# Kernel tuning notes

Measured on AMD Instinct MI355X. Metric: run time of the kernel, lower is better.

## Reference

```python
import jax, jax.numpy as jnp
import numpy as np
from jax.scipy.special import logsumexp

EPSILON = 0.01        # temperature
DIST_THRESH = 0.2
NUM_ITERS = 3
NEG_INF = -1.0e9

B, N, M, C = 4, 4096, 4096, 256


def setup_inputs() -> dict:
    key = jax.random.key(0)
    k1, k2, k3, k4, k5 = jax.random.split(key, 5)
    source_feats = jax.random.normal(k1, (B, N, C), dtype=jnp.float32)
    source_locs = jax.random.uniform(k2, (B, N, 2), dtype=jnp.float32)
    target_locs = jax.random.uniform(k3, (B, M, 2), dtype=jnp.float32)
    source_valid_mask = jax.random.bernoulli(k4, 0.9, (B, N))
    target_valid_mask = jax.random.bernoulli(k5, 0.9, (B, M))
    return {
        "source_feats": source_feats,
        "source_locs": source_locs,
        "target_locs": target_locs,
        "source_valid_mask": source_valid_mask,
        "target_valid_mask": target_valid_mask,
    }


def reference(source_feats, source_locs, target_locs, source_valid_mask, target_valid_mask):
    # pairwise squared distances: [B, M, N]
    diff = target_locs[:, :, None, :] - source_locs[:, None, :, :]  # [B, M, N, 2]
    dist_sq = jnp.sum(diff * diff, axis=-1)                          # [B, M, N]
    log_K = -dist_sq / (EPSILON + 1e-8)

    valid_connection = dist_sq < (DIST_THRESH ** 2)
    valid_connection = valid_connection & source_valid_mask[:, None, :]
    valid_connection = valid_connection & target_valid_mask[:, :, None]
    log_K = jnp.where(valid_connection, log_K, NEG_INF)

    # Sinkhorn iterations in log space
    v = jnp.zeros((log_K.shape[0], 1, log_K.shape[2]), dtype=log_K.dtype)  # [B,1,N]
    u = jnp.zeros((log_K.shape[0], log_K.shape[1], 1), dtype=log_K.dtype)  # [B,M,1]
    for _ in range(NUM_ITERS):
        u = -logsumexp(log_K + v, axis=2, keepdims=True)
        v = -logsumexp(log_K + u, axis=1, keepdims=True)
        v = jnp.where(source_valid_mask[:, None, :], v, 0.0)

    attn = jnp.exp(log_K + u + v)  # [B, M, N]
    attn = jax.lax.stop_gradient(attn)  # original computes it under torch.no_grad

    target_feats = jnp.einsum('bmn,bnc->bmc', attn, source_feats)
    target_feats = target_feats * target_valid_mask[:, :, None].astype(target_feats.dtype)
    has_source = jnp.any(valid_connection, axis=-1, keepdims=True)
    target_feats = target_feats * has_source.astype(target_feats.dtype)
    return target_feats
```

## Files before the change

kernel.cpp:

```cpp
#include <hip/hip_runtime.h>
#include <math.h>

#define BB 4
#define BN 4096
#define CC 256
constexpr float T2      = 0.04f;
constexpr float INV_EPS = (float)(1.0 / 0.01000001);

typedef __attribute__((ext_vector_type(8)))  short bf16x8;
typedef __attribute__((ext_vector_type(16))) float f32x16;

__device__ __forceinline__ int cell_of(float x, float y) {
  int cx = (int)(x * 5.0f); cx = cx < 0 ? 0 : (cx > 4 ? 4 : cx);
  int cy = (int)(y * 5.0f); cy = cy < 0 ? 0 : (cy > 4 ? 4 : cy);
  return cy * 5 + cx;
}

__device__ __forceinline__ void dma16(const void* g, void* l) {
  __builtin_amdgcn_global_load_lds(
      (const __attribute__((address_space(1))) void*)g,
      (__attribute__((address_space(3))) void*)l, 16, 0, 0);
}
__device__ __forceinline__ void dma4(const void* g, void* l) {
  __builtin_amdgcn_global_load_lds(
      (const __attribute__((address_space(1))) void*)g,
      (__attribute__((address_space(3))) void*)l, 4, 0, 0);
}

__global__ __launch_bounds__(256) void k_bin(
    const float* __restrict__ tlocs, const float* __restrict__ slocs,
    const int* __restrict__ tmask, const int* __restrict__ smask,
    int* __restrict__ Zc,
    int* __restrict__ starts_t, int* __restrict__ starts_s,
    int* __restrict__ perm_t, int* __restrict__ perm_s,
    float4* __restrict__ t_sorted, float4* __restrict__ s_sorted) {
  const int which = blockIdx.x & 1, b = blockIdx.x >> 1;
  const float* locs = which ? slocs : tlocs;
  const int*   mask = which ? smask : tmask;
  int* starts       = which ? starts_s : starts_t;
  int* perm         = which ? perm_s : perm_t;
  float4* pack      = which ? s_sorted : t_sorted;
  const int tid = threadIdx.x;
  if (blockIdx.x == 0) Zc[tid] = 0;
  __shared__ int cnt[25];
  __shared__ int st[26];
  __shared__ int cur[25];
  if (tid < 25) cnt[tid] = 0;
  __syncthreads();
  for (int i = tid; i < BN; i += 256)
    atomicAdd(&cnt[cell_of(locs[(b * BN + i) * 2], locs[(b * BN + i) * 2 + 1])], 1);
  __syncthreads();
  if (tid == 0) {
    int acc = 0;
    for (int c = 0; c < 25; c++) { st[c] = acc; acc += cnt[c]; }
    st[25] = acc;
  }
  __syncthreads();
  if (tid < 25) cur[tid] = st[tid];
  if (tid < 26) starts[b * 32 + tid] = st[tid];
  __syncthreads();
  for (int i = tid; i < BN; i += 256) {
    float x = locs[(b * BN + i) * 2], y = locs[(b * BN + i) * 2 + 1];
    int pos = atomicAdd(&cur[cell_of(x, y)], 1);
    perm[b * BN + pos] = i;
    pack[b * BN + pos] = make_float4(x, y, 0.f, mask[b * BN + i] ? 1.f : 0.f);
  }
}

__global__ __launch_bounds__(256) void k_pack(
    const float* __restrict__ feats, const int* __restrict__ perm_s,
    unsigned* __restrict__ fB) {
  const int b   = blockIdx.x >> 8;
  const int blk = blockIdx.x & 255;
  const int tid = threadIdx.x;
  __shared__ float fs[16][260];
  __shared__ int   sidx[16];
  if (tid < 16) sidx[tid] = perm_s[b * BN + blk * 16 + tid];
  __syncthreads();
  #pragma unroll
  for (int q = 0; q < 4; q++) {
    int idx = q * 256 + tid;
    int r = idx >> 6, c4 = idx & 63;
    float4 v = ((const float4*)feats)[(((b << 12) + sidx[r]) << 6) + c4];
    fs[r][c4 * 4 + 0] = v.x; fs[r][c4 * 4 + 1] = v.y;
    fs[r][c4 * 4 + 2] = v.z; fs[r][c4 * 4 + 3] = v.w;
  }
  __syncthreads();
  const int ch = tid;
  unsigned* dst = fB + ((((size_t)b << 8) + blk) << 12) + ch * 16;
  unsigned pk[16];
  #pragma unroll
  for (int sl = 0; sl < 16; sl++) {
    float f = fs[sl][ch];
    unsigned fb = __float_as_uint(f);
    unsigned hb = fb & 0xFFFF0000u;
    float lo = f - __uint_as_float(hb);
    pk[sl ^ (((ch >> 1) & 3) << 2)] = hb | (__float_as_uint(lo) >> 16);
  }
  #pragma unroll
  for (int q = 0; q < 4; q++)
    ((uint4*)dst)[q] = make_uint4(pk[q*4], pk[q*4+1], pk[q*4+2], pk[q*4+3]);
}

__global__ __launch_bounds__(256) void k_sink(const float4* __restrict__ opp,
                                              float4* __restrict__ own,
                                              const int* __restrict__ opp_starts,
                                              const int* __restrict__ Zin,
                                              int* __restrict__ Zout,
                                              int zero_invalid) {
  const int wv   = threadIdx.x >> 6;
  const int lane = threadIdx.x & 63;
  const int rowb = blockIdx.x * 16 + wv * 4;
  const int b    = rowb >> 12;
  float4 me[4];
  float  s[4] = {0.f, 0.f, 0.f, 0.f};
  int ryLo = 5, ryHi = -1, rxLo = 5, rxHi = -1;
  #pragma unroll
  for (int i = 0; i < 4; i++) {
    me[i] = own[rowb + i];
    if (me[i].w != 0.f) {
      int cell = cell_of(me[i].x, me[i].y);
      int cy = cell / 5, cx = cell % 5;
      ryLo = min(ryLo, max(cy - 1, 0)); ryHi = max(ryHi, min(cy + 1, 4));
      rxLo = min(rxLo, max(cx - 1, 0)); rxHi = max(rxHi, min(cx + 1, 4));
    }
  }
  for (int ry = ryLo; ry <= ryHi; ry++) {
    const int r0 = opp_starts[b * 32 + ry * 5 + rxLo];
    const int r1 = opp_starts[b * 32 + ry * 5 + rxHi + 1];
    for (int j = r0 + lane; j < r1; j += 64) {
      float4 o = opp[b * BN + j];
      #pragma unroll
      for (int i = 0; i < 4; i++) {
        float dx = me[i].x - o.x, dy = me[i].y - o.y;
        float d2 = fmaf(dx, dx, dy * dy);
        bool  c  = (d2 < T2) && (o.w != 0.f) && (me[i].w != 0.f);
        float t  = c ? fmaf(d2, -INV_EPS, o.z) : -3e30f;
        s[i] += __expf(t);
      }
    }
  }
  #pragma unroll
  for (int i = 0; i < 4; i++)
    for (int off = 32; off > 0; off >>= 1) s[i] += __shfl_xor(s[i], off);
  if (lane == 0) {
    const float Zf = (float)Zin[b];
    #pragma unroll
    for (int i = 0; i < 4; i++) {
      float ss  = s[i] + Zf;
      float val = (ss > 0.f) ? -logf(ss) : 1.0e9f;
      if (zero_invalid && me[i].w == 0.f) val = 0.f;
      own[rowb + i] = make_float4(me[i].x, me[i].y, val, me[i].w);
      if (val == 1.0e9f) atomicAdd(&Zout[b], 1);
    }
  }
}

#define MAXCH 12
#define BUFU  4352

__global__ __launch_bounds__(256) void k_out(
    const unsigned* __restrict__ fB, const float4* __restrict__ t_sorted,
    const float4* __restrict__ s_sorted, const int* __restrict__ perm_t,
    const int* __restrict__ starts_t, const int* __restrict__ starts_s,
    float* __restrict__ out) {
  const int b = blockIdx.z;
  const int cell = blockIdx.y / 3, rsel = blockIdx.y % 3;
  const int cy = cell / 5, cx = cell % 5;
  const int ry = cy + rsel - 1;
  if (ry < 0 || ry > 4) return;
  const int t0 = starts_t[b * 32 + cell], t1 = starts_t[b * 32 + cell + 1];
  const int base = t0 + blockIdx.x * 32;
  if (base >= t1) return;
  const int rx0 = max(cx - 1, 0), rx1 = min(cx + 1, 4);
  const int s0 = starts_s[b * 32 + ry * 5 + rx0];
  const int s1 = starts_s[b * 32 + ry * 5 + rx1 + 1];
  if (s0 >= s1) return;
  const int nt = min(32, t1 - base);

  __shared__ __align__(16) unsigned pool[3 * BUFU];
  __shared__ float4 tL[32];
  __shared__ int    morg[32];

  const int tid  = threadIdx.x;
  const int lane = tid & 63;
  const int w    = tid >> 6;

  if (tid < 32) {
    if (tid < nt) {
      tL[tid]   = t_sorted[b * BN + base + tid];
      morg[tid] = perm_t[b * BN + base + tid];
    } else {
      tL[tid]   = make_float4(0.f, 0.f, 0.f, 0.f);
      morg[tid] = 0;
    }
  }
  __syncthreads();

  const int kg = lane >> 5;
  const int ln = lane & 31;
  const float4 t4a = tL[ln];
  const int sB = b * BN;

  const int blk0 = s0 >> 4;
  const int nBlk = ((s1 + 15) >> 4) - blk0;

  const unsigned* fBb = fB + (((size_t)b) << 20);
  auto ISSUE = [&](int t, int bufI) {
    const unsigned* g = fBb + ((size_t)t << 12);
    unsigned* lb = pool + bufI * BUFU;
    #pragma unroll
    for (int q = 0; q < 4; q++)
      dma16(g + (w * 4 + q) * 256 + lane * 4, (void*)(lb + (w * 4 + q) * 256));
    dma4((const char*)s_sorted + ((size_t)(sB + t * 16) << 4) + lane * 4,
         (void*)(lb + 4096 + w * 64));
  };

  ISSUE(blk0, 0);
  ISSUE(blk0 + min(1, nBlk - 1), 1);

  f32x16 acc0, acc1;
  #pragma unroll
  for (int i = 0; i < 16; i++) { acc0[i] = 0.f; acc1[i] = 0.f; }

  int cur = 0;
  for (int r = 0; r < nBlk; r++) {
    asm volatile("s_waitcnt vmcnt(5)" ::: "memory");
    __builtin_amdgcn_sched_barrier(0);
    ISSUE(blk0 + min(r + 2, nBlk - 1), cur == 0 ? 2 : cur - 1);
    const unsigned* tile = pool + cur * BUFU;
    const int j0 = (blk0 + r) * 16 + kg * 8;
    unsigned ahv[8], alv[8];
    #pragma unroll
    for (int e = 0; e < 8; e++) {
      float4 s4 = *(const float4*)(tile + 4096 + w * 64 + (kg * 8 + e) * 4);
      int j = j0 + e;
      float dx = t4a.x - s4.x, dy = t4a.y - s4.y;
      float d2 = fmaf(dx, dx, dy * dy);
      bool  c  = (j >= s0) && (j < s1) && (d2 < T2) &&
                 (s4.w != 0.f) && (t4a.w != 0.f);
      float a  = c ? __expf(fmaf(d2, -INV_EPS, t4a.z + s4.z)) : 0.f;
      unsigned ab = __float_as_uint(a);
      unsigned hb = ab & 0xFFFF0000u;
      float alo = a - __uint_as_float(hb);
      ahv[e] = ab >> 16;
      alv[e] = __float_as_uint(alo) >> 16;
    }
    union { unsigned u[4]; bf16x8 v; } BH, BL;
    #pragma unroll
    for (int i = 0; i < 4; i++) {
      BH.u[i] = ahv[2*i] | (ahv[2*i+1] << 16);
      BL.u[i] = alv[2*i] | (alv[2*i+1] << 16);
    }
    #pragma unroll
    for (int mt = 0; mt < 2; mt++) {
      const int chl = w * 64 + mt * 32 + ln;
      const int xv  = (chl >> 1) & 3;
      const int g0  = ((kg << 1) | 0) ^ xv;
      const int g1  = ((kg << 1) | 1) ^ xv;
      union { uint4 q[2]; unsigned u[8]; } A;
      A.q[0] = *(const uint4*)(tile + chl * 16 + g0 * 4);
      A.q[1] = *(const uint4*)(tile + chl * 16 + g1 * 4);
      union { unsigned u[4]; bf16x8 v; } AH, AL;
      #pragma unroll
      for (int i = 0; i < 4; i++) {
        AH.u[i] = (A.u[2*i] >> 16)     | (A.u[2*i+1] & 0xFFFF0000u);
        AL.u[i] = (A.u[2*i] & 0xFFFFu) | (A.u[2*i+1] << 16);
      }
      if (mt == 0) {
        acc0 = __builtin_amdgcn_mfma_f32_32x32x16_bf16(AH.v, BH.v, acc0, 0, 0, 0);
        acc0 = __builtin_amdgcn_mfma_f32_32x32x16_bf16(AH.v, BL.v, acc0, 0, 0, 0);
        acc0 = __builtin_amdgcn_mfma_f32_32x32x16_bf16(AL.v, BH.v, acc0, 0, 0, 0);
      } else {
        acc1 = __builtin_amdgcn_mfma_f32_32x32x16_bf16(AH.v, BH.v, acc1, 0, 0, 0);
        acc1 = __builtin_amdgcn_mfma_f32_32x32x16_bf16(AH.v, BL.v, acc1, 0, 0, 0);
        acc1 = __builtin_amdgcn_mfma_f32_32x32x16_bf16(AL.v, BH.v, acc1, 0, 0, 0);
      }
    }
    cur = (cur == 2) ? 0 : cur + 1;
  }

  asm volatile("s_waitcnt vmcnt(0)" ::: "memory");
  __syncthreads();
  float* Dl = (float*)pool;
  #pragma unroll
  for (int mt = 0; mt < 2; mt++) {
    #pragma unroll
    for (int rg = 0; rg < 4; rg++) {
      int chb = w * 64 + mt * 32 + 8 * rg + 4 * kg;
      float4 v;
      if (mt == 0) v = make_float4(acc0[rg*4], acc0[rg*4+1], acc0[rg*4+2], acc0[rg*4+3]);
      else         v = make_float4(acc1[rg*4], acc1[rg*4+1], acc1[rg*4+2], acc1[rg*4+3]);
      *(float4*)&Dl[ln * 268 + chb] = v;
    }
  }
  __syncthreads();
  {
    const int tmg = tid >> 5, chg = tid & 31;
    #pragma unroll
    for (int i = 0; i < 4; i++) {
      int tm = tmg * 4 + i;
      if (tm < nt) {
        float* op = out + (((b << 12) + morg[tm]) << 8) + chg * 4;
        float4 d0 = *(float4*)&Dl[tm * 268 + chg * 4];
        float4 d1 = *(float4*)&Dl[tm * 268 + 128 + chg * 4];
        atomicAdd(op + 0, d0.x); atomicAdd(op + 1, d0.y);
        atomicAdd(op + 2, d0.z); atomicAdd(op + 3, d0.w);
        atomicAdd(op + 128, d1.x); atomicAdd(op + 129, d1.y);
        atomicAdd(op + 130, d1.z); atomicAdd(op + 131, d1.w);
      }
    }
  }
}

extern "C" void kernel_launch(void* const* d_in, const int* in_sizes, int n_in,
                              void* d_out, int out_size, void* d_ws, size_t ws_size,
                              hipStream_t stream) {
  const float* feats = (const float*)d_in[0];
  const float* slocs = (const float*)d_in[1];
  const float* tlocs = (const float*)d_in[2];
  const int*   smask = (const int*)d_in[3];
  const int*   tmask = (const int*)d_in[4];
  float* out = (float*)d_out;

  char* ws = (char*)d_ws;
  int*    Zc       = (int*)(ws + 1024);
  int*    starts_t = (int*)(ws + 2048);
  int*    starts_s = (int*)(ws + 2560);
  int*    perm_t   = (int*)(ws + 4096);
  int*    perm_s   = (int*)(ws + 69632);
  float4* s_sorted = (float4*)(ws + 135168);
  float4* t_sorted = (float4*)(ws + 397312);
  unsigned* fB     = (unsigned*)(ws + 663552);

  hipMemsetAsync(out, 0, (size_t)out_size * sizeof(float), stream);
  k_bin<<<8, 256, 0, stream>>>(tlocs, slocs, tmask, smask, Zc,
                               starts_t, starts_s, perm_t, perm_s,
                               t_sorted, s_sorted);
  k_pack<<<1024, 256, 0, stream>>>(feats, perm_s, fB);
  for (int it = 0; it < 3; it++) {
    k_sink<<<1024, 256, 0, stream>>>(s_sorted, t_sorted, starts_s,
                                     Zc + (it == 0 ? 0 : (2 * it) * 4),
                                     Zc + (2 * it + 1) * 4, 0);
    k_sink<<<1024, 256, 0, stream>>>(t_sorted, s_sorted, starts_t,
                                     Zc + (2 * it + 1) * 4,
                                     Zc + (2 * it + 2) * 4, 1);
  }
  k_out<<<dim3(MAXCH, 75, BB), 256, 0, stream>>>(fB, t_sorted, s_sorted,
                                                 perm_t, starts_t, starts_s,
                                                 out);
}
```

Baseline: 558.8 us.

## Use persistent work-queue k_out with 64-target tiles and simplify k_pack

k_out now processes 64 targets per work item with four accumulators, so each loaded source feature tile feeds twice as many MFMAs. It runs as a persistent grid of 768 blocks that take items from an atomic queue counter reset in k_bin, replacing the sparse 3D grid that had many early-exit blocks. k_pack drops its LDS staging and reads features directly. In exchange, register pressure rises, the output path adds an extra LDS round and barrier, and the queue serializes on one global atomic.

After: 552.9 us. Within noise of the previous version (-1.1%).

```diff
diff --git a/kernel.cpp b/kernel.cpp
--- a/kernel.cpp
+++ b/kernel.cpp
@@ -30,7 +30,7 @@
 __global__ __launch_bounds__(256) void k_bin(
     const float* __restrict__ tlocs, const float* __restrict__ slocs,
     const int* __restrict__ tmask, const int* __restrict__ smask,
-    int* __restrict__ Zc,
+    int* __restrict__ Zc, int* __restrict__ qcnt,
     int* __restrict__ starts_t, int* __restrict__ starts_s,
     int* __restrict__ perm_t, int* __restrict__ perm_s,
     float4* __restrict__ t_sorted, float4* __restrict__ s_sorted) {
@@ -41,7 +41,10 @@
   int* perm         = which ? perm_s : perm_t;
   float4* pack      = which ? s_sorted : t_sorted;
   const int tid = threadIdx.x;
-  if (blockIdx.x == 0) Zc[tid] = 0;
+  if (blockIdx.x == 0) {
+    Zc[tid] = 0;
+    if (tid == 0) qcnt[0] = 0;
+  }
   __shared__ int cnt[25];
   __shared__ int st[26];
   __shared__ int cur[25];
@@ -73,30 +76,20 @@
   const int b   = blockIdx.x >> 8;
   const int blk = blockIdx.x & 255;
   const int tid = threadIdx.x;
-  __shared__ float fs[16][260];
-  __shared__ int   sidx[16];
+  __shared__ int sidx[16];
   if (tid < 16) sidx[tid] = perm_s[b * BN + blk * 16 + tid];
   __syncthreads();
-  #pragma unroll
-  for (int q = 0; q < 4; q++) {
-    int idx = q * 256 + tid;
-    int r = idx >> 6, c4 = idx & 63;
-    float4 v = ((const float4*)feats)[(((b << 12) + sidx[r]) << 6) + c4];
-    fs[r][c4 * 4 + 0] = v.x; fs[r][c4 * 4 + 1] = v.y;
-    fs[r][c4 * 4 + 2] = v.z; fs[r][c4 * 4 + 3] = v.w;
-  }
-  __syncthreads();
   const int ch = tid;
-  unsigned* dst = fB + ((((size_t)b << 8) + blk) << 12) + ch * 16;
   unsigned pk[16];
   #pragma unroll
   for (int sl = 0; sl < 16; sl++) {
-    float f = fs[sl][ch];
-    unsigned fb = __float_as_uint(f);
-    unsigned hb = fb & 0xFFFF0000u;
+    float f = feats[((((size_t)(b << 12)) + sidx[sl]) << 8) + ch];
+    unsigned fbt = __float_as_uint(f);
+    unsigned hb  = fbt & 0xFFFF0000u;
     float lo = f - __uint_as_float(hb);
     pk[sl ^ (((ch >> 1) & 3) << 2)] = hb | (__float_as_uint(lo) >> 16);
   }
+  unsigned* dst = fB + ((((size_t)b << 8) + blk) << 12) + ch * 16;
   #pragma unroll
   for (int q = 0; q < 4; q++)
     ((uint4*)dst)[q] = make_uint4(pk[q*4], pk[q*4+1], pk[q*4+2], pk[q*4+3]);
@@ -156,159 +149,187 @@
   }
 }
 
-#define MAXCH 12
-#define BUFU  4352
+#define BUFU   4352
+#define NITEMS (BB * 25 * 3 * 6)
 
 __global__ __launch_bounds__(256) void k_out(
     const unsigned* __restrict__ fB, const float4* __restrict__ t_sorted,
     const float4* __restrict__ s_sorted, const int* __restrict__ perm_t,
     const int* __restrict__ starts_t, const int* __restrict__ starts_s,
-    float* __restrict__ out) {
-  const int b = blockIdx.z;
-  const int cell = blockIdx.y / 3, rsel = blockIdx.y % 3;
-  const int cy = cell / 5, cx = cell % 5;
-  const int ry = cy + rsel - 1;
-  if (ry < 0 || ry > 4) return;
-  const int t0 = starts_t[b * 32 + cell], t1 = starts_t[b * 32 + cell + 1];
-  const int base = t0 + blockIdx.x * 32;
-  if (base >= t1) return;
-  const int rx0 = max(cx - 1, 0), rx1 = min(cx + 1, 4);
-  const int s0 = starts_s[b * 32 + ry * 5 + rx0];
-  const int s1 = starts_s[b * 32 + ry * 5 + rx1 + 1];
-  if (s0 >= s1) return;
-  const int nt = min(32, t1 - base);
-
+    int* __restrict__ qcnt, float* __restrict__ out) {
   __shared__ __align__(16) unsigned pool[3 * BUFU];
-  __shared__ float4 tL[32];
-  __shared__ int    morg[32];
+  __shared__ float4 tL[64];
+  __shared__ int qi;
 
   const int tid  = threadIdx.x;
   const int lane = tid & 63;
   const int w    = tid >> 6;
-
-  if (tid < 32) {
-    if (tid < nt) {
-      tL[tid]   = t_sorted[b * BN + base + tid];
-      morg[tid] = perm_t[b * BN + base + tid];
-    } else {
-      tL[tid]   = make_float4(0.f, 0.f, 0.f, 0.f);
-      morg[tid] = 0;
-    }
-  }
-  __syncthreads();
-
-  const int kg = lane >> 5;
-  const int ln = lane & 31;
-  const float4 t4a = tL[ln];
-  const int sB = b * BN;
-
-  const int blk0 = s0 >> 4;
-  const int nBlk = ((s1 + 15) >> 4) - blk0;
-
-  const unsigned* fBb = fB + (((size_t)b) << 20);
-  auto ISSUE = [&](int t, int bufI) {
-    const unsigned* g = fBb + ((size_t)t << 12);
-    unsigned* lb = pool + bufI * BUFU;
+  const int kg   = lane >> 5;
+  const int ln   = lane & 31;
+
+  for (;;) {
+    if (tid == 0) qi = atomicAdd(qcnt, 1);
+    __syncthreads();
+    const int item = qi;
+    __syncthreads();
+    if (item >= NITEMS) break;
+    const int b    = item / 450;
+    const int r1_  = item % 450;
+    const int cell = r1_ / 18;
+    const int r2_  = r1_ % 18;
+    const int rsel = r2_ / 6, pair = r2_ % 6;
+    const int cy = cell / 5, cx = cell % 5;
+    const int ry = cy + rsel - 1;
+    if (ry < 0 || ry > 4) continue;
+    const int t0 = starts_t[b * 32 + cell], t1 = starts_t[b * 32 + cell + 1];
+    const int base = t0 + pair * 64;
+    if (base >= t1) continue;
+    const int rx0 = max(cx - 1, 0), rx1 = min(cx + 1, 4);
+    const int s0 = starts_s[b * 32 + ry * 5 + rx0];
+    const int s1 = starts_s[b * 32 + ry * 5 + rx1 + 1];
+    if (s0 >= s1) continue;
+    const int nt = min(64, t1 - base);
+
+    if (tid < 64)
+      tL[tid] = (tid < nt) ? t_sorted[b * BN + base + tid]
+                           : make_float4(0.f, 0.f, 0.f, 0.f);
+    __syncthreads();
+    const float4 t4a0 = tL[ln];
+    const float4 t4a1 = tL[32 + ln];
+    const int sB = b * BN;
+    const int blk0 = s0 >> 4;
+    const int nBlk = ((s1 + 15) >> 4) - blk0;
+
+    const unsigned* fBb = fB + (((size_t)b) << 20);
+    auto ISSUE = [&](int t, int bufI) {
+      const unsigned* g = fBb + ((size_t)t << 12);
+      unsigned* lb = pool + bufI * BUFU;
+      #pragma unroll
+      for (int q = 0; q < 4; q++)
+        dma16(g + (w * 4 + q) * 256 + lane * 4, (void*)(lb + (w * 4 + q) * 256));
+      dma4((const char*)s_sorted + ((size_t)(sB + t * 16) << 4) + lane * 4,
+           (void*)(lb + 4096 + w * 64));
+    };
+    ISSUE(blk0, 0);
+    ISSUE(blk0 + min(1, nBlk - 1), 1);
+
+    f32x16 a00, a01, a10, a11;
     #pragma unroll
-    for (int q = 0; q < 4; q++)
-      dma16(g + (w * 4 + q) * 256 + lane * 4, (void*)(lb + (w * 4 + q) * 256));
-    dma4((const char*)s_sorted + ((size_t)(sB + t * 16) << 4) + lane * 4,
-         (void*)(lb + 4096 + w * 64));
-  };
-
-  ISSUE(blk0, 0);
-  ISSUE(blk0 + min(1, nBlk - 1), 1);
-
-  f32x16 acc0, acc1;
-  #pragma unroll
-  for (int i = 0; i < 16; i++) { acc0[i] = 0.f; acc1[i] = 0.f; }
-
-  int cur = 0;
-  for (int r = 0; r < nBlk; r++) {
-    asm volatile("s_waitcnt vmcnt(5)" ::: "memory");
-    __builtin_amdgcn_sched_barrier(0);
-    ISSUE(blk0 + min(r + 2, nBlk - 1), cur == 0 ? 2 : cur - 1);
-    const unsigned* tile = pool + cur * BUFU;
-    const int j0 = (blk0 + r) * 16 + kg * 8;
-    unsigned ahv[8], alv[8];
+    for (int i = 0; i < 16; i++) { a00[i] = 0.f; a01[i] = 0.f; a10[i] = 0.f; a11[i] = 0.f; }
+
+    int cur = 0;
+    for (int r = 0; r < nBlk; r++) {
+      asm volatile("s_waitcnt vmcnt(5)" ::: "memory");
+      __builtin_amdgcn_sched_barrier(0);
+      ISSUE(blk0 + min(r + 2, nBlk - 1), cur == 0 ? 2 : cur - 1);
+      const unsigned* tile = pool + cur * BUFU;
+      const int j0 = (blk0 + r) * 16 + kg * 8;
+      unsigned ah0[8], al0[8], ah1[8], al1[8];
+      #pragma unroll
+      for (int e = 0; e < 8; e++) {
+        float4 s4 = *(const float4*)(tile + 4096 + w * 64 + (kg * 8 + e) * 4);
+        int j = j0 + e;
+        bool inr = (j >= s0) && (j < s1) && (s4.w != 0.f);
+        float dx0 = t4a0.x - s4.x, dy0 = t4a0.y - s4.y;
+        float d20 = fmaf(dx0, dx0, dy0 * dy0);
+        bool  c0  = inr && (d20 < T2) && (t4a0.w != 0.f);
+        float a0  = c0 ? __expf(fmaf(d20, -INV_EPS, t4a0.z + s4.z)) : 0.f;
+        unsigned ab0 = __float_as_uint(a0);
+        unsigned hb0 = ab0 & 0xFFFF0000u;
+        float alo0 = a0 - __uint_as_float(hb0);
+        ah0[e] = ab0 >> 16; al0[e] = __float_as_uint(alo0) >> 16;
+        float dx1 = t4a1.x - s4.x, dy1 = t4a1.y - s4.y;
+        float d21 = fmaf(dx1, dx1, dy1 * dy1);
+        bool  c1  = inr && (d21 < T2) && (t4a1.w != 0.f);
+        float a1  = c1 ? __expf(fmaf(d21, -INV_EPS, t4a1.z + s4.z)) : 0.f;
+        unsigned ab1 = __float_as_uint(a1);
+        unsigned hb1 = ab1 & 0xFFFF0000u;
+        float alo1 = a1 - __uint_as_float(hb1);
+        ah1[e] = ab1 >> 16; al1[e] = __float_as_uint(alo1) >> 16;
+      }
+      union { unsigned u[4]; bf16x8 v; } BH0, BL0, BH1, BL1;
+      #pragma unroll
+      for (int i = 0; i < 4; i++) {
+        BH0.u[i] = ah0[2*i] | (ah0[2*i+1] << 16);
+        BL0.u[i] = al0[2*i] | (al0[2*i+1] << 16);
+        BH1.u[i] = ah1[2*i] | (ah1[2*i+1] << 16);
+        BL1.u[i] = al1[2*i] | (al1[2*i+1] << 16);
+      }
+      #pragma unroll
+      for (int mt = 0; mt < 2; mt++) {
+        const int chl = w * 64 + mt * 32 + ln;
+        const int xv  = (chl >> 1) & 3;
+        const int g0  = ((kg << 1) | 0) ^ xv;
+        const int g1  = ((kg << 1) | 1) ^ xv;
+        union { uint4 q[2]; unsigned u[8]; } A;
+        A.q[0] = *(const uint4*)(tile + chl * 16 + g0 * 4);
+        A.q[1] = *(const uint4*)(tile + chl * 16 + g1 * 4);
+        union { unsigned u[4]; bf16x8 v; } AH, AL;
+        #pragma unroll
+        for (int i = 0; i < 4; i++) {
+          AH.u[i] = (A.u[2*i] >> 16)     | (A.u[2*i+1] & 0xFFFF0000u);
+          AL.u[i] = (A.u[2*i] & 0xFFFFu) | (A.u[2*i+1] << 16);
+        }
+        if (mt == 0) {
+          a00 = __builtin_amdgcn_mfma_f32_32x32x16_bf16(AH.v, BH0.v, a00, 0, 0, 0);
+          a00 = __builtin_amdgcn_mfma_f32_32x32x16_bf16(AH.v, BL0.v, a00, 0, 0, 0);
+          a00 = __builtin_amdgcn_mfma_f32_32x32x16_bf16(AL.v, BH0.v, a00, 0, 0, 0);
+          a10 = __builtin_amdgcn_mfma_f32_32x32x16_bf16(AH.v, BH1.v, a10, 0, 0, 0);
+          a10 = __builtin_amdgcn_mfma_f32_32x32x16_bf16(AH.v, BL1.v, a10, 0, 0, 0);
+          a10 = __builtin_amdgcn_mfma_f32_32x32x16_bf16(AL.v, BH1.v, a10, 0, 0, 0);
+        } else {
+          a01 = __builtin_amdgcn_mfma_f32_32x32x16_bf16(AH.v, BH0.v, a01, 0, 0, 0);
+          a01 = __builtin_amdgcn_mfma_f32_32x32x16_bf16(AH.v, BL0.v, a01, 0, 0, 0);
+          a01 = __builtin_amdgcn_mfma_f32_32x32x16_bf16(AL.v, BH0.v, a01, 0, 0, 0);
+          a11 = __builtin_amdgcn_mfma_f32_32x32x16_bf16(AH.v, BH1.v, a11, 0, 0, 0);
+          a11 = __builtin_amdgcn_mfma_f32_32x32x16_bf16(AH.v, BL1.v, a11, 0, 0, 0);
+          a11 = __builtin_amdgcn_mfma_f32_32x32x16_bf16(AL.v, BH1.v, a11, 0, 0, 0);
+        }
+      }
+      cur = (cur == 2) ? 0 : cur + 1;
+    }
+
+    asm volatile("s_waitcnt vmcnt(0)" ::: "memory");
+    __syncthreads();
+    float* Dl = (float*)pool;
     #pragma unroll
-    for (int e = 0; e < 8; e++) {
-      float4 s4 = *(const float4*)(tile + 4096 + w * 64 + (kg * 8 + e) * 4);
-      int j = j0 + e;
-      float dx = t4a.x - s4.x, dy = t4a.y - s4.y;
-      float d2 = fmaf(dx, dx, dy * dy);
-      bool  c  = (j >= s0) && (j < s1) && (d2 < T2) &&
-                 (s4.w != 0.f) && (t4a.w != 0.f);
-      float a  = c ? __expf(fmaf(d2, -INV_EPS, t4a.z + s4.z)) : 0.f;
-      unsigned ab = __float_as_uint(a);
-      unsigned hb = ab & 0xFFFF0000u;
-      float alo = a - __uint_as_float(hb);
-      ahv[e] = ab >> 16;
-      alv[e] = __float_as_uint(alo) >> 16;
-    }
-    union { unsigned u[4]; bf16x8 v; } BH, BL;
-    #pragma unroll
-    for (int i = 0; i < 4; i++) {
-      BH.u[i] = ahv[2*i] | (ahv[2*i+1] << 16);
-      BL.u[i] = alv[2*i] | (alv[2*i+1] << 16);
-    }
-    #pragma unroll
-    for (int mt = 0; mt < 2; mt++) {
-      const int chl = w * 64 + mt * 32 + ln;
-      const int xv  = (chl >> 1) & 3;
-      const int g0  = ((kg << 1) | 0) ^ xv;
-      const int g1  = ((kg << 1) | 1) ^ xv;
-      union { uint4 q[2]; unsigned u[8]; } A;
-      A.q[0] = *(const uint4*)(tile + chl * 16 + g0 * 4);
-      A.q[1] = *(const uint4*)(tile + chl * 16 + g1 * 4);
-      union { unsigned u[4]; bf16x8 v; } AH, AL;
-      #pragma unroll
-      for (int i = 0; i < 4; i++) {
-        AH.u[i] = (A.u[2*i] >> 16)     | (A.u[2*i+1] & 0xFFFF0000u);
-        AL.u[i] = (A.u[2*i] & 0xFFFFu) | (A.u[2*i+1] << 16);
-      }
-      if (mt == 0) {
-        acc0 = __builtin_amdgcn_mfma_f32_32x32x16_bf16(AH.v, BH.v, acc0, 0, 0, 0);
-        acc0 = __builtin_amdgcn_mfma_f32_32x32x16_bf16(AH.v, BL.v, acc0, 0, 0, 0);
-        acc0 = __builtin_amdgcn_mfma_f32_32x32x16_bf16(AL.v, BH.v, acc0, 0, 0, 0);
-      } else {
-        acc1 = __builtin_amdgcn_mfma_f32_32x32x16_bf16(AH.v, BH.v, acc1, 0, 0, 0);
-        acc1 = __builtin_amdgcn_mfma_f32_32x32x16_bf16(AH.v, BL.v, acc1, 0, 0, 0);
-        acc1 = __builtin_amdgcn_mfma_f32_32x32x16_bf16(AL.v, BH.v, acc1, 0, 0, 0);
-      }
-    }
-    cur = (cur == 2) ? 0 : cur + 1;
-  }
-
-  asm volatile("s_waitcnt vmcnt(0)" ::: "memory");
-  __syncthreads();
-  float* Dl = (float*)pool;
-  #pragma unroll
-  for (int mt = 0; mt < 2; mt++) {
-    #pragma unroll
-    for (int rg = 0; rg < 4; rg++) {
-      int chb = w * 64 + mt * 32 + 8 * rg + 4 * kg;
-      float4 v;
-      if (mt == 0) v = make_float4(acc0[rg*4], acc0[rg*4+1], acc0[rg*4+2], acc0[rg*4+3]);
-      else         v = make_float4(acc1[rg*4], acc1[rg*4+1], acc1[rg*4+2], acc1[rg*4+3]);
-      *(float4*)&Dl[ln * 268 + chb] = v;
-    }
-  }
-  __syncthreads();
-  {
-    const int tmg = tid >> 5, chg = tid & 31;
-    #pragma unroll
-    for (int i = 0; i < 4; i++) {
-      int tm = tmg * 4 + i;
-      if (tm < nt) {
-        float* op = out + (((b << 12) + morg[tm]) << 8) + chg * 4;
-        float4 d0 = *(float4*)&Dl[tm * 268 + chg * 4];
-        float4 d1 = *(float4*)&Dl[tm * 268 + 128 + chg * 4];
-        atomicAdd(op + 0, d0.x); atomicAdd(op + 1, d0.y);
-        atomicAdd(op + 2, d0.z); atomicAdd(op + 3, d0.w);
-        atomicAdd(op + 128, d1.x); atomicAdd(op + 129, d1.y);
-        atomicAdd(op + 130, d1.z); atomicAdd(op + 131, d1.w);
-      }
+    for (int c = 0; c < 2; c++) {
+      #pragma unroll
+      for (int mt = 0; mt < 2; mt++) {
+        #pragma unroll
+        for (int rg = 0; rg < 4; rg++) {
+          int chb = w * 64 + mt * 32 + 8 * rg + 4 * kg;
+          float4 v;
+          if (c == 0) {
+            if (mt == 0) v = make_float4(a00[rg*4], a00[rg*4+1], a00[rg*4+2], a00[rg*4+3]);
+            else         v = make_float4(a01[rg*4], a01[rg*4+1], a01[rg*4+2], a01[rg*4+3]);
+          } else {
+            if (mt == 0) v = make_float4(a10[rg*4], a10[rg*4+1], a10[rg*4+2], a10[rg*4+3]);
+            else         v = make_float4(a11[rg*4], a11[rg*4+1], a11[rg*4+2], a11[rg*4+3]);
+          }
+          *(float4*)&Dl[ln * 268 + chb] = v;
+        }
+      }
+      __syncthreads();
+      {
+        const int tmg = tid >> 5, chg = tid & 31;
+        #pragma unroll
+        for (int i = 0; i < 4; i++) {
+          int tm = tmg * 4 + i;
+          int gt = c * 32 + tm;
+          if (gt < nt) {
+            int row = perm_t[sB + base + gt];
+            float* op = out + (((b << 12) + row) << 8) + chg * 4;
+            float4 d0 = *(float4*)&Dl[tm * 268 + chg * 4];
+            float4 d1 = *(float4*)&Dl[tm * 268 + 128 + chg * 4];
+            atomicAdd(op + 0, d0.x); atomicAdd(op + 1, d0.y);
+            atomicAdd(op + 2, d0.z); atomicAdd(op + 3, d0.w);
+            atomicAdd(op + 128, d1.x); atomicAdd(op + 129, d1.y);
+            atomicAdd(op + 130, d1.z); atomicAdd(op + 131, d1.w);
+          }
+        }
+      }
+      __syncthreads();
     }
   }
 }
@@ -324,6 +345,7 @@
   float* out = (float*)d_out;
 
   char* ws = (char*)d_ws;
+  int*    qcnt     = (int*)(ws);
   int*    Zc       = (int*)(ws + 1024);
   int*    starts_t = (int*)(ws + 2048);
   int*    starts_s = (int*)(ws + 2560);
@@ -334,7 +356,7 @@
   unsigned* fB     = (unsigned*)(ws + 663552);
 
   hipMemsetAsync(out, 0, (size_t)out_size * sizeof(float), stream);
-  k_bin<<<8, 256, 0, stream>>>(tlocs, slocs, tmask, smask, Zc,
+  k_bin<<<8, 256, 0, stream>>>(tlocs, slocs, tmask, smask, Zc, qcnt,
                                starts_t, starts_s, perm_t, perm_s,
                                t_sorted, s_sorted);
   k_pack<<<1024, 256, 0, stream>>>(feats, perm_s, fB);
@@ -346,7 +368,6 @@
                                      Zc + (2 * it + 1) * 4,
                                      Zc + (2 * it + 2) * 4, 1);
   }
-  k_out<<<dim3(MAXCH, 75, BB), 256, 0, stream>>>(fB, t_sorted, s_sorted,
-                                                 perm_t, starts_t, starts_s,
-                                                 out);
-}
+  k_out<<<768, 256, 0, stream>>>(fB, t_sorted, s_sorted, perm_t,
+                                 starts_t, starts_s, qcnt, out);
+}
```

## Make k_out a persistent work-queue kernel with direct register loads of features

Applied to the files above, without the earlier changes.

k_out becomes a persistent kernel: 1024 blocks pull work items from an atomic counter that k_bin resets. Feature tiles are now loaded from global memory straight into registers with one-tile register prefetch, replacing the LDS triple buffer filled by global_load_lds. k_pack drops its LDS staging and XOR swizzle and reads features directly. The goal is less LDS traffic and better load balance across uneven cell workloads. The cost is a global atomic per item, extra barriers, uncoalesced feature reads in k_pack, and reliance on L1/L2 for the per-lane s_sorted loads.

Result: no change. 559.0 us (+0.0%).

```diff
diff --git a/kernel.cpp b/kernel.cpp
--- a/kernel.cpp
+++ b/kernel.cpp
@@ -16,21 +16,10 @@
   return cy * 5 + cx;
 }
 
-__device__ __forceinline__ void dma16(const void* g, void* l) {
-  __builtin_amdgcn_global_load_lds(
-      (const __attribute__((address_space(1))) void*)g,
-      (__attribute__((address_space(3))) void*)l, 16, 0, 0);
-}
-__device__ __forceinline__ void dma4(const void* g, void* l) {
-  __builtin_amdgcn_global_load_lds(
-      (const __attribute__((address_space(1))) void*)g,
-      (__attribute__((address_space(3))) void*)l, 4, 0, 0);
-}
-
 __global__ __launch_bounds__(256) void k_bin(
     const float* __restrict__ tlocs, const float* __restrict__ slocs,
     const int* __restrict__ tmask, const int* __restrict__ smask,
-    int* __restrict__ Zc,
+    int* __restrict__ Zc, int* __restrict__ qcnt,
     int* __restrict__ starts_t, int* __restrict__ starts_s,
     int* __restrict__ perm_t, int* __restrict__ perm_s,
     float4* __restrict__ t_sorted, float4* __restrict__ s_sorted) {
@@ -41,7 +30,10 @@
   int* perm         = which ? perm_s : perm_t;
   float4* pack      = which ? s_sorted : t_sorted;
   const int tid = threadIdx.x;
-  if (blockIdx.x == 0) Zc[tid] = 0;
+  if (blockIdx.x == 0) {
+    Zc[tid] = 0;
+    if (tid == 0) qcnt[0] = 0;
+  }
   __shared__ int cnt[25];
   __shared__ int st[26];
   __shared__ int cur[25];
@@ -73,30 +65,20 @@
   const int b   = blockIdx.x >> 8;
   const int blk = blockIdx.x & 255;
   const int tid = threadIdx.x;
-  __shared__ float fs[16][260];
-  __shared__ int   sidx[16];
+  __shared__ int sidx[16];
   if (tid < 16) sidx[tid] = perm_s[b * BN + blk * 16 + tid];
   __syncthreads();
-  #pragma unroll
-  for (int q = 0; q < 4; q++) {
-    int idx = q * 256 + tid;
-    int r = idx >> 6, c4 = idx & 63;
-    float4 v = ((const float4*)feats)[(((b << 12) + sidx[r]) << 6) + c4];
-    fs[r][c4 * 4 + 0] = v.x; fs[r][c4 * 4 + 1] = v.y;
-    fs[r][c4 * 4 + 2] = v.z; fs[r][c4 * 4 + 3] = v.w;
-  }
-  __syncthreads();
   const int ch = tid;
-  unsigned* dst = fB + ((((size_t)b << 8) + blk) << 12) + ch * 16;
   unsigned pk[16];
   #pragma unroll
   for (int sl = 0; sl < 16; sl++) {
-    float f = fs[sl][ch];
-    unsigned fb = __float_as_uint(f);
-    unsigned hb = fb & 0xFFFF0000u;
+    float f = feats[((((size_t)(b << 12)) + sidx[sl]) << 8) + ch];
+    unsigned fbt = __float_as_uint(f);
+    unsigned hb  = fbt & 0xFFFF0000u;
     float lo = f - __uint_as_float(hb);
-    pk[sl ^ (((ch >> 1) & 3) << 2)] = hb | (__float_as_uint(lo) >> 16);
-  }
+    pk[sl] = hb | (__float_as_uint(lo) >> 16);
+  }
+  unsigned* dst = fB + ((((size_t)b << 8) + blk) << 12) + ch * 16;
   #pragma unroll
   for (int q = 0; q < 4; q++)
     ((uint4*)dst)[q] = make_uint4(pk[q*4], pk[q*4+1], pk[q*4+2], pk[q*4+3]);
@@ -156,158 +138,156 @@
   }
 }
 
-#define MAXCH 12
-#define BUFU  4352
-
-__global__ __launch_bounds__(256) void k_out(
+#define NITEMS (BB * 25 * 3 * 12)
+
+__global__ __launch_bounds__(256, 4) void k_out(
     const unsigned* __restrict__ fB, const float4* __restrict__ t_sorted,
     const float4* __restrict__ s_sorted, const int* __restrict__ perm_t,
     const int* __restrict__ starts_t, const int* __restrict__ starts_s,
-    float* __restrict__ out) {
-  const int b = blockIdx.z;
-  const int cell = blockIdx.y / 3, rsel = blockIdx.y % 3;
-  const int cy = cell / 5, cx = cell % 5;
-  const int ry = cy + rsel - 1;
-  if (ry < 0 || ry > 4) return;
-  const int t0 = starts_t[b * 32 + cell], t1 = starts_t[b * 32 + cell + 1];
-  const int base = t0 + blockIdx.x * 32;
-  if (base >= t1) return;
-  const int rx0 = max(cx - 1, 0), rx1 = min(cx + 1, 4);
-  const int s0 = starts_s[b * 32 + ry * 5 + rx0];
-  const int s1 = starts_s[b * 32 + ry * 5 + rx1 + 1];
-  if (s0 >= s1) return;
-  const int nt = min(32, t1 - base);
-
-  __shared__ __align__(16) unsigned pool[3 * BUFU];
+    int* __restrict__ qcnt, float* __restrict__ out) {
   __shared__ float4 tL[32];
-  __shared__ int    morg[32];
+  __shared__ __align__(16) float Dl[32 * 268];
+  __shared__ int qi;
 
   const int tid  = threadIdx.x;
   const int lane = tid & 63;
   const int w    = tid >> 6;
-
-  if (tid < 32) {
-    if (tid < nt) {
-      tL[tid]   = t_sorted[b * BN + base + tid];
-      morg[tid] = perm_t[b * BN + base + tid];
-    } else {
-      tL[tid]   = make_float4(0.f, 0.f, 0.f, 0.f);
-      morg[tid] = 0;
-    }
-  }
-  __syncthreads();
-
-  const int kg = lane >> 5;
-  const int ln = lane & 31;
-  const float4 t4a = tL[ln];
-  const int sB = b * BN;
-
-  const int blk0 = s0 >> 4;
-  const int nBlk = ((s1 + 15) >> 4) - blk0;
-
-  const unsigned* fBb = fB + (((size_t)b) << 20);
-  auto ISSUE = [&](int t, int bufI) {
-    const unsigned* g = fBb + ((size_t)t << 12);
-    unsigned* lb = pool + bufI * BUFU;
+  const int kg   = lane >> 5;
+  const int ln   = lane & 31;
+
+  for (;;) {
+    if (tid == 0) qi = atomicAdd(qcnt, 1);
+    __syncthreads();
+    const int item = qi;
+    __syncthreads();
+    if (item >= NITEMS) break;
+    const int b    = item / 900;
+    const int r1_  = item % 900;
+    const int cell = r1_ / 36;
+    const int r2_  = r1_ % 36;
+    const int rsel = r2_ / 12, chunk = r2_ % 12;
+    const int cy = cell / 5, cx = cell % 5;
+    const int ry = cy + rsel - 1;
+    if (ry < 0 || ry > 4) continue;
+    const int t0 = starts_t[b * 32 + cell], t1 = starts_t[b * 32 + cell + 1];
+    const int base = t0 + chunk * 32;
+    if (base >= t1) continue;
+    const int rx0 = max(cx - 1, 0), rx1 = min(cx + 1, 4);
+    const int s0 = starts_s[b * 32 + ry * 5 + rx0];
+    const int s1 = starts_s[b * 32 + ry * 5 + rx1 + 1];
+    if (s0 >= s1) continue;
+    const int nt = min(32, t1 - base);
+
+    if (tid < 32)
+      tL[tid] = (tid < nt) ? t_sorted[b * BN + base + tid]
+                           : make_float4(0.f, 0.f, 0.f, 0.f);
+    __syncthreads();
+    const float4 t4a = tL[ln];
+    const int sB = b * BN;
+    const int blk0 = s0 >> 4;
+    const int nBlk = ((s1 + 15) >> 4) - blk0;
+
+    const unsigned* fBb = fB + (((size_t)b) << 20);
+    const int aoff0 = (w * 64 + ln) * 16 + kg * 8;
+    const int aoff1 = aoff0 + 512;
+
+    const unsigned* g0p = fBb + ((size_t)blk0 << 12);
+    uint4 cA00 = *(const uint4*)(g0p + aoff0);
+    uint4 cA01 = *(const uint4*)(g0p + aoff0 + 4);
+    uint4 cA10 = *(const uint4*)(g0p + aoff1);
+    uint4 cA11 = *(const uint4*)(g0p + aoff1 + 4);
+
+    f32x16 acc0, acc1;
     #pragma unroll
-    for (int q = 0; q < 4; q++)
-      dma16(g + (w * 4 + q) * 256 + lane * 4, (void*)(lb + (w * 4 + q) * 256));
-    dma4((const char*)s_sorted + ((size_t)(sB + t * 16) << 4) + lane * 4,
-         (void*)(lb + 4096 + w * 64));
-  };
-
-  ISSUE(blk0, 0);
-  ISSUE(blk0 + min(1, nBlk - 1), 1);
-
-  f32x16 acc0, acc1;
-  #pragma unroll
-  for (int i = 0; i < 16; i++) { acc0[i] = 0.f; acc1[i] = 0.f; }
-
-  int cur = 0;
-  for (int r = 0; r < nBlk; r++) {
-    asm volatile("s_waitcnt vmcnt(5)" ::: "memory");
-    __builtin_amdgcn_sched_barrier(0);
-    ISSUE(blk0 + min(r + 2, nBlk - 1), cur == 0 ? 2 : cur - 1);
-    const unsigned* tile = pool + cur * BUFU;
-    const int j0 = (blk0 + r) * 16 + kg * 8;
-    unsigned ahv[8], alv[8];
-    #pragma unroll
-    for (int e = 0; e < 8; e++) {
-      float4 s4 = *(const float4*)(tile + 4096 + w * 64 + (kg * 8 + e) * 4);
-      int j = j0 + e;
-      float dx = t4a.x - s4.x, dy = t4a.y - s4.y;
-      float d2 = fmaf(dx, dx, dy * dy);
-      bool  c  = (j >= s0) && (j < s1) && (d2 < T2) &&
-                 (s4.w != 0.f) && (t4a.w != 0.f);
-      float a  = c ? __expf(fmaf(d2, -INV_EPS, t4a.z + s4.z)) : 0.f;
-      unsigned ab = __float_as_uint(a);
-      unsigned hb = ab & 0xFFFF0000u;
-      float alo = a - __uint_as_float(hb);
-      ahv[e] = ab >> 16;
-      alv[e] = __float_as_uint(alo) >> 16;
-    }
-    union { unsigned u[4]; bf16x8 v; } BH, BL;
-    #pragma unroll
-    for (int i = 0; i < 4; i++) {
-      BH.u[i] = ahv[2*i] | (ahv[2*i+1] << 16);
-      BL.u[i] = alv[2*i] | (alv[2*i+1] << 16);
-    }
+    for (int i = 0; i < 16; i++) { acc0[i] = 0.f; acc1[i] = 0.f; }
+
+    for (int r = 0; r < nBlk; r++) {
+      const int tn = blk0 + min(r + 1, nBlk - 1);
+      const unsigned* gn = fBb + ((size_t)tn << 12);
+      uint4 nA00 = *(const uint4*)(gn + aoff0);
+      uint4 nA01 = *(const uint4*)(gn + aoff0 + 4);
+      uint4 nA10 = *(const uint4*)(gn + aoff1);
+      uint4 nA11 = *(const uint4*)(gn + aoff1 + 4);
+      const int j0 = (blk0 + r) * 16 + kg * 8;
+      float4 s4v[8];
+      #pragma unroll
+      for (int e = 0; e < 8; e++)
+        s4v[e] = s_sorted[sB + j0 + e];
+      union { unsigned u[4]; bf16x8 v; } BH, BL;
+      #pragma unroll
+      for (int i = 0; i < 4; i++) {
+        unsigned hh[2], ll[2];
+        #pragma unroll
+        for (int p = 0; p < 2; p++) {
+          const int e = 2 * i + p;
+          float4 s4 = s4v[e];
+          int j = j0 + e;
+          float dx = t4a.x - s4.x, dy = t4a.y - s4.y;
+          float d2 = fmaf(dx, dx, dy * dy);
+          bool  c  = (j >= s0) && (j < s1) && (d2 < T2) &&
+                     (s4.w != 0.f) && (t4a.w != 0.f);
+          float a  = c ? __expf(fmaf(d2, -INV_EPS, t4a.z + s4.z)) : 0.f;
+          unsigned ab = __float_as_uint(a);
+          unsigned hb = ab & 0xFFFF0000u;
+          float alo = a - __uint_as_float(hb);
+          hh[p] = ab >> 16;
+          ll[p] = __float_as_uint(alo) >> 16;
+        }
+        BH.u[i] = hh[0] | (hh[1] << 16);
+        BL.u[i] = ll[0] | (ll[1] << 16);
+      }
+      #pragma unroll
+      for (int mt = 0; mt < 2; mt++) {
+        union { uint4 q[2]; unsigned u[8]; } A;
+        A.q[0] = (mt == 0) ? cA00 : cA10;
+        A.q[1] = (mt == 0) ? cA01 : cA11;
+        union { unsigned u[4]; bf16x8 v; } AH, AL;
+        #pragma unroll
+        for (int i = 0; i < 4; i++) {
+          AH.u[i] = (A.u[2*i] >> 16)     | (A.u[2*i+1] & 0xFFFF0000u);
+          AL.u[i] = (A.u[2*i] & 0xFFFFu) | (A.u[2*i+1] << 16);
+        }
+        if (mt == 0) {
+          acc0 = __builtin_amdgcn_mfma_f32_32x32x16_bf16(AH.v, BH.v, acc0, 0, 0, 0);
+          acc0 = __builtin_amdgcn_mfma_f32_32x32x16_bf16(AH.v, BL.v, acc0, 0, 0, 0);
+          acc0 = __builtin_amdgcn_mfma_f32_32x32x16_bf16(AL.v, BH.v, acc0, 0, 0, 0);
+        } else {
+          acc1 = __builtin_amdgcn_mfma_f32_32x32x16_bf16(AH.v, BH.v, acc1, 0, 0, 0);
+          acc1 = __builtin_amdgcn_mfma_f32_32x32x16_bf16(AH.v, BL.v, acc1, 0, 0, 0);
+          acc1 = __builtin_amdgcn_mfma_f32_32x32x16_bf16(AL.v, BH.v, acc1, 0, 0, 0);
+        }
+      }
+      cA00 = nA00; cA01 = nA01; cA10 = nA10; cA11 = nA11;
+    }
+
+    __syncthreads();
     #pragma unroll
     for (int mt = 0; mt < 2; mt++) {
-      const int chl = w * 64 + mt * 32 + ln;
-      const int xv  = (chl >> 1) & 3;
-      const int g0  = ((kg << 1) | 0) ^ xv;
-      const int g1  = ((kg << 1) | 1) ^ xv;
-      union { uint4 q[2]; unsigned u[8]; } A;
-      A.q[0] = *(const uint4*)(tile + chl * 16 + g0 * 4);
-      A.q[1] = *(const uint4*)(tile + chl * 16 + g1 * 4);
-      union { unsigned u[4]; bf16x8 v; } AH, AL;
+      #pragma unroll
+      for (int rg = 0; rg < 4; rg++) {
+        int chb = w * 64 + mt * 32 + 8 * rg + 4 * kg;
+        float4 v;
+        if (mt == 0) v = make_float4(acc0[rg*4], acc0[rg*4+1], acc0[rg*4+2], acc0[rg*4+3]);
+        else         v = make_float4(acc1[rg*4], acc1[rg*4+1], acc1[rg*4+2], acc1[rg*4+3]);
+        *(float4*)&Dl[ln * 268 + chb] = v;
+      }
+    }
+    __syncthreads();
+    {
+      const int tmg = tid >> 5, chg = tid & 31;
       #pragma unroll
       for (int i = 0; i < 4; i++) {
-        AH.u[i] = (A.u[2*i] >> 16)     | (A.u[2*i+1] & 0xFFFF0000u);
-        AL.u[i] = (A.u[2*i] & 0xFFFFu) | (A.u[2*i+1] << 16);
-      }
-      if (mt == 0) {
-        acc0 = __builtin_amdgcn_mfma_f32_32x32x16_bf16(AH.v, BH.v, acc0, 0, 0, 0);
-        acc0 = __builtin_amdgcn_mfma_f32_32x32x16_bf16(AH.v, BL.v, acc0, 0, 0, 0);
-        acc0 = __builtin_amdgcn_mfma_f32_32x32x16_bf16(AL.v, BH.v, acc0, 0, 0, 0);
-      } else {
-        acc1 = __builtin_amdgcn_mfma_f32_32x32x16_bf16(AH.v, BH.v, acc1, 0, 0, 0);
-        acc1 = __builtin_amdgcn_mfma_f32_32x32x16_bf16(AH.v, BL.v, acc1, 0, 0, 0);
-        acc1 = __builtin_amdgcn_mfma_f32_32x32x16_bf16(AL.v, BH.v, acc1, 0, 0, 0);
-      }
-    }
-    cur = (cur == 2) ? 0 : cur + 1;
-  }
-
-  asm volatile("s_waitcnt vmcnt(0)" ::: "memory");
-  __syncthreads();
-  float* Dl = (float*)pool;
-  #pragma unroll
-  for (int mt = 0; mt < 2; mt++) {
-    #pragma unroll
-    for (int rg = 0; rg < 4; rg++) {
-      int chb = w * 64 + mt * 32 + 8 * rg + 4 * kg;
-      float4 v;
-      if (mt == 0) v = make_float4(acc0[rg*4], acc0[rg*4+1], acc0[rg*4+2], acc0[rg*4+3]);
-      else         v = make_float4(acc1[rg*4], acc1[rg*4+1], acc1[rg*4+2], acc1[rg*4+3]);
-      *(float4*)&Dl[ln * 268 + chb] = v;
-    }
-  }
-  __syncthreads();
-  {
-    const int tmg = tid >> 5, chg = tid & 31;
-    #pragma unroll
-    for (int i = 0; i < 4; i++) {
-      int tm = tmg * 4 + i;
-      if (tm < nt) {
-        float* op = out + (((b << 12) + morg[tm]) << 8) + chg * 4;
-        float4 d0 = *(float4*)&Dl[tm * 268 + chg * 4];
-        float4 d1 = *(float4*)&Dl[tm * 268 + 128 + chg * 4];
-        atomicAdd(op + 0, d0.x); atomicAdd(op + 1, d0.y);
-        atomicAdd(op + 2, d0.z); atomicAdd(op + 3, d0.w);
-        atomicAdd(op + 128, d1.x); atomicAdd(op + 129, d1.y);
-        atomicAdd(op + 130, d1.z); atomicAdd(op + 131, d1.w);
+        int tm = tmg * 4 + i;
+        if (tm < nt) {
+          int row = perm_t[sB + base + tm];
+          float* op = out + (((b << 12) + row) << 8) + chg * 4;
+          float4 d0 = *(float4*)&Dl[tm * 268 + chg * 4];
+          float4 d1 = *(float4*)&Dl[tm * 268 + 128 + chg * 4];
+          atomicAdd(op + 0, d0.x); atomicAdd(op + 1, d0.y);
+          atomicAdd(op + 2, d0.z); atomicAdd(op + 3, d0.w);
+          atomicAdd(op + 128, d1.x); atomicAdd(op + 129, d1.y);
+          atomicAdd(op + 130, d1.z); atomicAdd(op + 131, d1.w);
+        }
       }
     }
   }
@@ -324,6 +304,7 @@
   float* out = (float*)d_out;
 
   char* ws = (char*)d_ws;
+  int*    qcnt     = (int*)(ws);
   int*    Zc       = (int*)(ws + 1024);
   int*    starts_t = (int*)(ws + 2048);
   int*    starts_s = (int*)(ws + 2560);
@@ -334,7 +315,7 @@
   unsigned* fB     = (unsigned*)(ws + 663552);
 
   hipMemsetAsync(out, 0, (size_t)out_size * sizeof(float), stream);
-  k_bin<<<8, 256, 0, stream>>>(tlocs, slocs, tmask, smask, Zc,
+  k_bin<<<8, 256, 0, stream>>>(tlocs, slocs, tmask, smask, Zc, qcnt,
                                starts_t, starts_s, perm_t, perm_s,
                                t_sorted, s_sorted);
   k_pack<<<1024, 256, 0, stream>>>(feats, perm_s, fB);
@@ -346,7 +327,6 @@
                                      Zc + (2 * it + 1) * 4,
                                      Zc + (2 * it + 2) * 4, 1);
   }
-  k_out<<<dim3(MAXCH, 75, BB), 256, 0, stream>>>(fB, t_sorted, s_sorted,
-                                                 perm_t, starts_t, starts_s,
-                                                 out);
-}
+  k_out<<<1024, 256, 0, stream>>>(fB, t_sorted, s_sorted, perm_t,
+                                  starts_t, starts_s, qcnt, out);
+}
```
